# Kernel tuning notes

Hardware: AMD Instinct MI355X
Metric: run time of the kernel (lower is better)

The kernel has to match this reference:

```python
import jax, jax.numpy as jnp
import numpy as np

S, N, E = 4, 50000, 800000
DIM_C, DIM_H, HID = 8, 8, 32


def _mlp(x, W1, b1, W2, b2):
    # MLP(dim_in, dim_out, dim_hidden, num_hidden=1, CELU): lin -> celu -> lin
    return jax.nn.celu(x @ W1 + b1) @ W2 + b2


def setup_inputs() -> dict:
    key = jax.random.key(0)
    ks = jax.random.split(key, 12)

    def lin(k, fan_in, fan_out):
        kw, kb = jax.random.split(k)
        s = 1.0 / np.sqrt(fan_in)
        W = jax.random.uniform(kw, (fan_in, fan_out), jnp.float32, -s, s)
        b = jax.random.uniform(kb, (fan_out,), jnp.float32, -s, s)
        return W, b

    dz = DIM_C + DIM_H
    cur_W1, cur_b1 = lin(ks[0], dz, HID)
    cur_W2, cur_b2 = lin(ks[1], HID, HID)
    nbr_W1, nbr_b1 = lin(ks[2], dz, HID)
    nbr_W2, nbr_b2 = lin(ks[3], HID, HID)
    out_W, out_b = lin(ks[4], 2 * HID, DIM_C)
    G_W1, G_b1 = lin(ks[5], DIM_C, HID)
    G_W2, G_b2 = lin(ks[6], HID, DIM_H)

    z = jax.random.normal(ks[7], (S, N, dz), jnp.float32)
    src = jax.random.randint(ks[8], (E,), 0, N, jnp.int32)
    dst = jax.random.randint(ks[9], (E,), 0, N, jnp.int32)
    t = jnp.zeros((1,), jnp.float32)

    return dict(t=t, z=z, src=src, dst=dst,
                cur_W1=cur_W1, cur_b1=cur_b1, cur_W2=cur_W2, cur_b2=cur_b2,
                nbr_W1=nbr_W1, nbr_b1=nbr_b1, nbr_W2=nbr_W2, nbr_b2=nbr_b2,
                out_W=out_W, out_b=out_b,
                G_W1=G_W1, G_b1=G_b1, G_W2=G_W2, G_b2=G_b2)


def reference(t, z, src, dst,
              cur_W1, cur_b1, cur_W2, cur_b2,
              nbr_W1, nbr_b1, nbr_W2, nbr_b2,
              out_W, out_b,
              G_W1, G_b1, G_W2, G_b2):
    # z: [S, N, dim_c + dim_h]
    c = z[..., :DIM_C]          # [S, N, dim_c]
    h = z[..., DIM_C:]          # [S, N, dim_h]

    # GCU: vcur = act(MLP(z_node)); vnbr = sum over neighbors of act(MLP(z_nbr))
    vcur = jax.nn.celu(_mlp(z, cur_W1, cur_b1, cur_W2, cur_b2))      # [S, N, HID]
    vnbr_all = jax.nn.celu(_mlp(z, nbr_W1, nbr_b1, nbr_W2, nbr_b2))  # [S, N, HID]
    # segment-sum neighbor messages over edge list (nodes with no neighbors get zeros)
    agg = jnp.zeros((S, N, HID), z.dtype).at[:, dst].add(vnbr_all[:, src])  # [S, N, HID]

    dc = jnp.tanh(jnp.concatenate([vcur, agg], axis=-1) @ out_W + out_b)   # [S, N, dim_c]
    # project dc onto the tangent space orthogonal to c (sphere constraint)
    dc = dc - (dc * c).sum(axis=2, keepdims=True) / (c * c).sum(axis=2, keepdims=True) * c

    # gated decay of h
    G = jax.nn.softplus(_mlp(c, G_W1, G_b1, G_W2, G_b2))  # [S, N, dim_h]
    dh = -G * h

    return jnp.concatenate([dc, dh], axis=2)
```

## Files before the change

kernel.cpp:

```cpp
#include <hip/hip_runtime.h>

#define S_ 4
#define N_ 50000
#define E_ 800000
#define DIM_C 8
#define DIM_H 8
#define HID 32
#define DZ 16
#define CAP 64
#define NPART 6250
#define ECHUNK 2048
#define NCHUNK ((E_ + ECHUNK - 1) / ECHUNK)

typedef unsigned int u32;
typedef unsigned short u16;
typedef __attribute__((ext_vector_type(8))) short short8;
typedef __attribute__((ext_vector_type(4))) float f32x4;

__device__ __forceinline__ float celu_f(float x) {
    return x > 0.f ? x : __expf(x) - 1.f;
}
__device__ __forceinline__ float tanh_f(float x) {
    float e = __expf(-2.f * fabsf(x));
    float r = (1.f - e) * __builtin_amdgcn_rcpf(1.f + e);
    return copysignf(r, x);
}
__device__ __forceinline__ float softplus_f(float x) {
    return fmaxf(x, 0.f) + __logf(1.f + __expf(-fabsf(x)));
}
__device__ __forceinline__ u16 f2bf(float f) {
    u32 x = __float_as_uint(f);
    return (u16)((x + 0x7fffu + ((x >> 16) & 1u)) >> 16);
}
__device__ __forceinline__ float bf2f(u16 v) {
    return __uint_as_float(((u32)v) << 16);
}

#define MFMA(a, b, c) __builtin_amdgcn_mfma_f32_16x16x32_bf16(a, b, c, 0, 0, 0)

#define CNT_IDX(n) ((size_t)(n) << 5)
#define CNT_INT4S (N_ * 32 / 4)

__global__ __launch_bounds__(256) void zero_prep_kernel(
    const float* __restrict__ cW1, const float* __restrict__ cW2,
    const float* __restrict__ nW1, const float* __restrict__ nW2,
    const float* __restrict__ gW1, const float* __restrict__ gW2,
    const float* __restrict__ oW,
    u16* __restrict__ frags, int* __restrict__ cnt)
{
    if (blockIdx.x >= 13) {
        u32 i = (blockIdx.x - 13) * 256 + threadIdx.x;
        if (i < CNT_INT4S) {
            int4 zz; zz.x = 0; zz.y = 0; zz.z = 0; zz.w = 0;
            ((int4*)cnt)[i] = zz;
        }
        return;
    }
    if (threadIdx.x >= 64) return;
    int tile = blockIdx.x;
    int lane = threadIdx.x;
    int cl = lane & 15, g = lane >> 4;
    #pragma unroll
    for (int j = 0; j < 8; ++j) {
        int k = 8 * g + j;
        float v = 0.f;
        switch (tile) {
            case 0:  v = (k < DZ)    ? cW1[k*HID + cl]      : 0.f; break;
            case 1:  v = (k < DZ)    ? cW1[k*HID + cl + 16] : 0.f; break;
            case 2:  v = cW2[k*HID + cl];                          break;
            case 3:  v = cW2[k*HID + cl + 16];                     break;
            case 4:  v = (k < DZ)    ? nW1[k*HID + cl]      : 0.f; break;
            case 5:  v = (k < DZ)    ? nW1[k*HID + cl + 16] : 0.f; break;
            case 6:  v = nW2[k*HID + cl];                          break;
            case 7:  v = nW2[k*HID + cl + 16];                     break;
            case 8:  v = (k < DIM_C) ? gW1[k*HID + cl]      : 0.f; break;
            case 9:  v = (k < DIM_C) ? gW1[k*HID + cl + 16] : 0.f; break;
            case 10: v = (cl < DIM_H)? gW2[k*DIM_H + cl]    : 0.f; break;
            case 11: v = (cl < DIM_C)? oW[k*DIM_C + cl]        : 0.f; break;
            case 12: v = (cl < DIM_C)? oW[(HID+k)*DIM_C + cl]  : 0.f; break;
        }
        frags[((size_t)tile * 64 + lane) * 8 + j] = f2bf(v);
    }
}

__global__ __launch_bounds__(256) void node_fill_kernel(
    const float* __restrict__ z, const u16* __restrict__ frags,
    const float* __restrict__ cb1, const float* __restrict__ cb2,
    const float* __restrict__ nb1, const float* __restrict__ nb2,
    const float* __restrict__ gb1, const float* __restrict__ gb2,
    const float* __restrict__ ob,
    u16* __restrict__ pcd, u16* __restrict__ ub,
    const int* __restrict__ src, const int* __restrict__ dst,
    int* __restrict__ cnt, u16* __restrict__ list)
{
    __shared__ __align__(16) u16 sh[4][16][40];

    int m = blockIdx.x >> 4;
    int j = blockIdx.x & 15;

    if (j < 8) {
        int plo = j * NPART, phi = plo + NPART;
        int e0 = m * ECHUNK + (int)threadIdx.x * 8;
        if (e0 < E_) {
            int4 da = *(const int4*)(dst + e0);
            int4 db = *(const int4*)(dst + e0 + 4);
            int4 sa = *(const int4*)(src + e0);
            int4 sb = *(const int4*)(src + e0 + 4);
            int dv[8] = {da.x, da.y, da.z, da.w, db.x, db.y, db.z, db.w};
            int sv[8] = {sa.x, sa.y, sa.z, sa.w, sb.x, sb.y, sb.z, sb.w};
            #pragma unroll
            for (int i = 0; i < 8; ++i) {
                int dn = dv[i];
                if (dn >= plo && dn < phi) {
                    int pos = atomicAdd(&cnt[CNT_IDX(dn)], 1);
                    if (pos < CAP) list[(size_t)dn * CAP + pos] = (u16)sv[i];
                }
            }
        }
        return;
    }

    int g = m * 8 + (j - 8);
    if (g >= 3125) return;
    int w    = threadIdx.x >> 6;
    int lane = threadIdx.x & 63;
    int s = w;
    int base = g * 16;

    int r  = lane & 15;
    int gg = lane >> 4;
    int k0 = 8 * gg;

    const short8* F = (const short8*)frags;
    short8 bW1c_lo = F[0*64+lane],  bW1c_hi = F[1*64+lane];
    short8 bW2c_lo = F[2*64+lane],  bW2c_hi = F[3*64+lane];
    short8 bW1n_lo = F[4*64+lane],  bW1n_hi = F[5*64+lane];
    short8 bW2n_lo = F[6*64+lane],  bW2n_hi = F[7*64+lane];
    short8 bG1_lo  = F[8*64+lane],  bG1_hi  = F[9*64+lane];
    short8 bG2_lo  = F[10*64+lane];
    short8 bOWc    = F[11*64+lane], bOWn    = F[12*64+lane];

    int cl = r;
    float bc1lo = cb1[cl], bc1hi = cb1[cl+16];
    float bc2lo = cb2[cl], bc2hi = cb2[cl+16];
    float bn1lo = nb1[cl], bn1hi = nb1[cl+16];
    float bn2lo = nb2[cl], bn2hi = nb2[cl+16];
    float bg1lo = gb1[cl], bg1hi = gb1[cl+16];
    float bg2v  = (cl < 8) ? gb2[cl] : 0.f;
    float obv   = (cl < 8) ? ob[cl]  : 0.f;

    const f32x4 zero4 = {0.f, 0.f, 0.f, 0.f};

    int rowbase = s * N_ + base;

    short8 a1 = {0,0,0,0,0,0,0,0};
    if (gg < 2) {
        const float* zp = z + (size_t)(rowbase + r) * DZ + k0;
        float4 x = *(const float4*)zp;
        float4 y = *(const float4*)(zp + 4);
        a1[0]=(short)f2bf(x.x); a1[1]=(short)f2bf(x.y); a1[2]=(short)f2bf(x.z); a1[3]=(short)f2bf(x.w);
        a1[4]=(short)f2bf(y.x); a1[5]=(short)f2bf(y.y); a1[6]=(short)f2bf(y.z); a1[7]=(short)f2bf(y.w);
    }

    {
        f32x4 d0 = MFMA(a1, bW1c_lo, zero4);
        f32x4 d1 = MFMA(a1, bW1c_hi, zero4);
        #pragma unroll
        for (int q = 0; q < 4; ++q) {
            sh[w][4*gg+q][cl]    = f2bf(celu_f(d0[q] + bc1lo));
            sh[w][4*gg+q][cl+16] = f2bf(celu_f(d1[q] + bc1hi));
        }
        short8 a2 = *(const short8*)&sh[w][r][k0];
        d0 = MFMA(a2, bW2c_lo, zero4);
        d1 = MFMA(a2, bW2c_hi, zero4);
        #pragma unroll
        for (int q = 0; q < 4; ++q) {
            sh[w][4*gg+q][cl]    = f2bf(celu_f(d0[q] + bc2lo));
            sh[w][4*gg+q][cl+16] = f2bf(celu_f(d1[q] + bc2hi));
        }
        short8 a2v = *(const short8*)&sh[w][r][k0];
        f32x4 dp = MFMA(a2v, bOWc, zero4);
        if (cl < 8) {
            #pragma unroll
            for (int q = 0; q < 4; ++q)
                sh[w][4*gg+q][32 + cl] = f2bf(dp[q] + obv);
        }
        if (gg == 0) {
            uint4 vv = *(const uint4*)&sh[w][r][32];
            *(uint4*)(pcd + (size_t)(base + r) * 64 + s * 16) = vv;
        }
    }

    {
        f32x4 d0 = MFMA(a1, bW1n_lo, zero4);
        f32x4 d1 = MFMA(a1, bW1n_hi, zero4);
        #pragma unroll
        for (int q = 0; q < 4; ++q) {
            sh[w][4*gg+q][cl]    = f2bf(celu_f(d0[q] + bn1lo));
            sh[w][4*gg+q][cl+16] = f2bf(celu_f(d1[q] + bn1hi));
        }
        short8 a2 = *(const short8*)&sh[w][r][k0];
        d0 = MFMA(a2, bW2n_lo, zero4);
        d1 = MFMA(a2, bW2n_hi, zero4);
        #pragma unroll
        for (int q = 0; q < 4; ++q) {
            sh[w][4*gg+q][cl]    = f2bf(celu_f(d0[q] + bn2lo));
            sh[w][4*gg+q][cl+16] = f2bf(celu_f(d1[q] + bn2hi));
        }
        short8 a2n = *(const short8*)&sh[w][r][k0];
        f32x4 du = MFMA(a2n, bOWn, zero4);
        if (cl < 8) {
            #pragma unroll
            for (int q = 0; q < 4; ++q)
                sh[w][4*gg+q][32 + cl] = f2bf(du[q]);
        }
        if (gg == 0) {
            uint4 vv = *(const uint4*)&sh[w][r][32];
            *(uint4*)(ub + (size_t)(base + r) * 32 + s * 8) = vv;
        }
    }

    {
        f32x4 d0 = MFMA(a1, bG1_lo, zero4);
        f32x4 d1 = MFMA(a1, bG1_hi, zero4);
        #pragma unroll
        for (int q = 0; q < 4; ++q) {
            sh[w][4*gg+q][cl]    = f2bf(celu_f(d0[q] + bg1lo));
            sh[w][4*gg+q][cl+16] = f2bf(celu_f(d1[q] + bg1hi));
        }
        short8 a2 = *(const short8*)&sh[w][r][k0];
        f32x4 dG = MFMA(a2, bG2_lo, zero4);
        if (cl < 8) {
            #pragma unroll
            for (int q = 0; q < 4; ++q) {
                int mm = rowbase + 4*gg + q;
                float gv = softplus_f(dG[q] + bg2v);
                float hs = z[(size_t)mm * DZ + DIM_C + cl];
                sh[w][4*gg+q][32 + cl] = f2bf(-gv * hs);
            }
        }
        if (gg == 0) {
            uint4 vv = *(const uint4*)&sh[w][r][32];
            *(uint4*)(pcd + (size_t)(base + r) * 64 + s * 16 + 8) = vv;
        }
    }
}

__global__ __launch_bounds__(256) void gather_final_kernel(
    const u16* __restrict__ list, const int* __restrict__ cnt,
    const u16* __restrict__ ub, const u16* __restrict__ pcd,
    const float* __restrict__ z,
    float* __restrict__ out)
{
    int n = blockIdx.x * 4 + (threadIdx.x >> 6);
    int lane = threadIdx.x & 63;
    if (n >= N_) return;
    int deg = cnt[CNT_IDX(n)];
    deg = deg < CAP ? deg : CAP;
    int lv = (int)list[(size_t)n * CAP + lane];
    int half = lane >> 5;
    int ll = lane & 31;

    float sum = 0.f;
    int e = 0;
    for (; e + 7 < deg; e += 8) {
        int m0 = e + half;
        int s0 = __shfl(lv, m0);
        int s1 = __shfl(lv, m0 + 2);
        int s2 = __shfl(lv, m0 + 4);
        int s3 = __shfl(lv, m0 + 6);
        sum += bf2f(ub[(size_t)s0 * 32 + ll]);
        sum += bf2f(ub[(size_t)s1 * 32 + ll]);
        sum += bf2f(ub[(size_t)s2 * 32 + ll]);
        sum += bf2f(ub[(size_t)s3 * 32 + ll]);
    }
    for (; e < deg; e += 2) {
        int me = e + half;
        int sn = __shfl(lv, me & 63);
        if (me < deg) sum += bf2f(ub[(size_t)sn * 32 + ll]);
    }
    sum += __shfl_xor(sum, 32);

    if (half == 0) {
        int s = ll >> 3, j = ll & 7;
        int row = s * N_ + n;
        float pre = bf2f(pcd[(size_t)n * 64 + s * 16 + j]) + sum;
        float dc = tanh_f(pre);
        float c = z[(size_t)row * DZ + j];
        float num = dc * c, den = c * c;
        num += __shfl_xor(num, 1); den += __shfl_xor(den, 1);
        num += __shfl_xor(num, 2); den += __shfl_xor(den, 2);
        num += __shfl_xor(num, 4); den += __shfl_xor(den, 4);
        float coef = num * __builtin_amdgcn_rcpf(den);
        out[(size_t)row * DZ + j] = fmaf(-coef, c, dc);
        out[(size_t)row * DZ + DIM_C + j] = bf2f(pcd[(size_t)n * 64 + s * 16 + 8 + j]);
    }
}

extern "C" void kernel_launch(void* const* d_in, const int* in_sizes, int n_in,
                              void* d_out, int out_size, void* d_ws, size_t ws_size,
                              hipStream_t stream) {
    const float* z      = (const float*)d_in[1];
    const int*   src    = (const int*)  d_in[2];
    const int*   dst    = (const int*)  d_in[3];
    const float* cur_W1 = (const float*)d_in[4];
    const float* cur_b1 = (const float*)d_in[5];
    const float* cur_W2 = (const float*)d_in[6];
    const float* cur_b2 = (const float*)d_in[7];
    const float* nbr_W1 = (const float*)d_in[8];
    const float* nbr_b1 = (const float*)d_in[9];
    const float* nbr_W2 = (const float*)d_in[10];
    const float* nbr_b2 = (const float*)d_in[11];
    const float* out_W  = (const float*)d_in[12];
    const float* out_b  = (const float*)d_in[13];
    const float* G_W1   = (const float*)d_in[14];
    const float* G_b1   = (const float*)d_in[15];
    const float* G_W2   = (const float*)d_in[16];
    const float* G_b2   = (const float*)d_in[17];
    float* out = (float*)d_out;

    u16* ub    = (u16*)d_ws;
    u16* pcd   = ub + (size_t)N_ * 32;
    u16* list  = pcd + (size_t)N_ * 64;
    int* cnt   = (int*)(list + (size_t)N_ * CAP);
    u16* frags = (u16*)(cnt + (size_t)N_ * 32);

    int ZB = 13 + (CNT_INT4S + 255) / 256;
    zero_prep_kernel<<<ZB, 256, 0, stream>>>(
        cur_W1, cur_W2, nbr_W1, nbr_W2, G_W1, G_W2, out_W, frags, cnt);

    node_fill_kernel<<<NCHUNK * 16, 256, 0, stream>>>(
        z, frags,
        cur_b1, cur_b2, nbr_b1, nbr_b2, G_b1, G_b2, out_b,
        pcd, ub, src, dst, cnt, list);

    gather_final_kernel<<<(N_ + 3) / 4, 256, 0, stream>>>(
        list, cnt, ub, pcd, z, out);
}
```

Measured before the change: 73.08 us.

## Pre-bucket edges by destination partition to avoid redundant per-partition edge scans

Adds an edge-compaction phase to the prep kernel that buckets each 2048-edge chunk by destination partition in shared memory and writes packed (local dst, src) words to a global staging buffer. The scatter blocks in node_fill now read only their partition's entries instead of all edges in the chunk eightfold. This cuts redundant src/dst reads and branch-filtered work, at the cost of an extra staging write/read and moving edge work into the earlier kernel. Buckets are capped at 512 entries, which silently drops edges if a partition overflows.

```diff
diff --git a/kernel.cpp b/kernel.cpp
--- a/kernel.cpp
+++ b/kernel.cpp
@@ -11,6 +11,8 @@
 #define NPART 6250
 #define ECHUNK 2048
 #define NCHUNK ((E_ + ECHUNK - 1) / ECHUNK)
+#define STCAP 512
+#define ZEROB ((N_ * 32 / 4 + 255) / 256)
 
 typedef unsigned int u32;
 typedef unsigned short u16;
@@ -41,45 +43,85 @@
 #define CNT_IDX(n) ((size_t)(n) << 5)
 #define CNT_INT4S (N_ * 32 / 4)
 
-__global__ __launch_bounds__(256) void zero_prep_kernel(
+__global__ __launch_bounds__(256) void zero_prep_compact_kernel(
     const float* __restrict__ cW1, const float* __restrict__ cW2,
     const float* __restrict__ nW1, const float* __restrict__ nW2,
     const float* __restrict__ gW1, const float* __restrict__ gW2,
     const float* __restrict__ oW,
-    u16* __restrict__ frags, int* __restrict__ cnt)
+    const int* __restrict__ src, const int* __restrict__ dst,
+    u16* __restrict__ frags, int* __restrict__ cnt,
+    u32* __restrict__ stage, int* __restrict__ acount)
 {
-    if (blockIdx.x >= 13) {
-        u32 i = (blockIdx.x - 13) * 256 + threadIdx.x;
+    __shared__ u32 buck[8][STCAP];
+    __shared__ int bcnt[8];
+    const int bid = blockIdx.x;
+    const int tid = threadIdx.x;
+
+    if (bid < 13) {
+        if (tid >= 64) return;
+        int tile = bid;
+        int cl = tid & 15, g = tid >> 4;
+        #pragma unroll
+        for (int j = 0; j < 8; ++j) {
+            int k = 8 * g + j;
+            float v = 0.f;
+            switch (tile) {
+                case 0:  v = (k < DZ)    ? cW1[k*HID + cl]      : 0.f; break;
+                case 1:  v = (k < DZ)    ? cW1[k*HID + cl + 16] : 0.f; break;
+                case 2:  v = cW2[k*HID + cl];                          break;
+                case 3:  v = cW2[k*HID + cl + 16];                     break;
+                case 4:  v = (k < DZ)    ? nW1[k*HID + cl]      : 0.f; break;
+                case 5:  v = (k < DZ)    ? nW1[k*HID + cl + 16] : 0.f; break;
+                case 6:  v = nW2[k*HID + cl];                          break;
+                case 7:  v = nW2[k*HID + cl + 16];                     break;
+                case 8:  v = (k < DIM_C) ? gW1[k*HID + cl]      : 0.f; break;
+                case 9:  v = (k < DIM_C) ? gW1[k*HID + cl + 16] : 0.f; break;
+                case 10: v = (cl < DIM_H)? gW2[k*DIM_H + cl]    : 0.f; break;
+                case 11: v = (cl < DIM_C)? oW[k*DIM_C + cl]        : 0.f; break;
+                case 12: v = (cl < DIM_C)? oW[(HID+k)*DIM_C + cl]  : 0.f; break;
+            }
+            frags[((size_t)tile * 64 + tid) * 8 + j] = f2bf(v);
+        }
+        return;
+    }
+
+    if (bid < 13 + ZEROB) {
+        u32 i = (u32)(bid - 13) * 256 + tid;
         if (i < CNT_INT4S) {
             int4 zz; zz.x = 0; zz.y = 0; zz.z = 0; zz.w = 0;
             ((int4*)cnt)[i] = zz;
         }
         return;
     }
-    if (threadIdx.x >= 64) return;
-    int tile = blockIdx.x;
-    int lane = threadIdx.x;
-    int cl = lane & 15, g = lane >> 4;
+
+    int m = bid - (13 + ZEROB);
+    if (tid < 8) bcnt[tid] = 0;
+    __syncthreads();
+    int e0 = m * ECHUNK + tid * 8;
+    if (e0 < E_) {
+        int4 da = *(const int4*)(dst + e0);
+        int4 db = *(const int4*)(dst + e0 + 4);
+        int4 sa = *(const int4*)(src + e0);
+        int4 sb = *(const int4*)(src + e0 + 4);
+        int dv[8] = {da.x, da.y, da.z, da.w, db.x, db.y, db.z, db.w};
+        int sv[8] = {sa.x, sa.y, sa.z, sa.w, sb.x, sb.y, sb.z, sb.w};
+        #pragma unroll
+        for (int i = 0; i < 8; ++i) {
+            int dn = dv[i];
+            int p = dn / NPART;
+            int slot = atomicAdd(&bcnt[p], 1);
+            if (slot < STCAP)
+                buck[p][slot] = (u32)(dn - p * NPART) | ((u32)sv[i] << 16);
+        }
+    }
+    __syncthreads();
     #pragma unroll
-    for (int j = 0; j < 8; ++j) {
-        int k = 8 * g + j;
-        float v = 0.f;
-        switch (tile) {
-            case 0:  v = (k < DZ)    ? cW1[k*HID + cl]      : 0.f; break;
-            case 1:  v = (k < DZ)    ? cW1[k*HID + cl + 16] : 0.f; break;
-            case 2:  v = cW2[k*HID + cl];                          break;
-            case 3:  v = cW2[k*HID + cl + 16];                     break;
-            case 4:  v = (k < DZ)    ? nW1[k*HID + cl]      : 0.f; break;
-            case 5:  v = (k < DZ)    ? nW1[k*HID + cl + 16] : 0.f; break;
-            case 6:  v = nW2[k*HID + cl];                          break;
-            case 7:  v = nW2[k*HID + cl + 16];                     break;
-            case 8:  v = (k < DIM_C) ? gW1[k*HID + cl]      : 0.f; break;
-            case 9:  v = (k < DIM_C) ? gW1[k*HID + cl + 16] : 0.f; break;
-            case 10: v = (cl < DIM_H)? gW2[k*DIM_H + cl]    : 0.f; break;
-            case 11: v = (cl < DIM_C)? oW[k*DIM_C + cl]        : 0.f; break;
-            case 12: v = (cl < DIM_C)? oW[(HID+k)*DIM_C + cl]  : 0.f; break;
-        }
-        frags[((size_t)tile * 64 + lane) * 8 + j] = f2bf(v);
+    for (int p = 0; p < 8; ++p) {
+        int c = bcnt[p];
+        c = c < STCAP ? c : STCAP;
+        u32* sg = stage + ((size_t)m * 8 + p) * STCAP;
+        for (int i = tid; i < c; i += 256) sg[i] = buck[p][i];
+        if (tid == 0) acount[m * 8 + p] = c;
     }
 }
 
@@ -90,7 +132,7 @@
     const float* __restrict__ gb1, const float* __restrict__ gb2,
     const float* __restrict__ ob,
     u16* __restrict__ pcd, u16* __restrict__ ub,
-    const int* __restrict__ src, const int* __restrict__ dst,
+    const u32* __restrict__ stage, const int* __restrict__ acount,
     int* __restrict__ cnt, u16* __restrict__ list)
 {
     __shared__ __align__(16) u16 sh[4][16][40];
@@ -99,23 +141,15 @@
     int j = blockIdx.x & 15;
 
     if (j < 8) {
-        int plo = j * NPART, phi = plo + NPART;
-        int e0 = m * ECHUNK + (int)threadIdx.x * 8;
-        if (e0 < E_) {
-            int4 da = *(const int4*)(dst + e0);
-            int4 db = *(const int4*)(dst + e0 + 4);
-            int4 sa = *(const int4*)(src + e0);
-            int4 sb = *(const int4*)(src + e0 + 4);
-            int dv[8] = {da.x, da.y, da.z, da.w, db.x, db.y, db.z, db.w};
-            int sv[8] = {sa.x, sa.y, sa.z, sa.w, sb.x, sb.y, sb.z, sb.w};
-            #pragma unroll
-            for (int i = 0; i < 8; ++i) {
-                int dn = dv[i];
-                if (dn >= plo && dn < phi) {
-                    int pos = atomicAdd(&cnt[CNT_IDX(dn)], 1);
-                    if (pos < CAP) list[(size_t)dn * CAP + pos] = (u16)sv[i];
-                }
-            }
+        int c = acount[m * 8 + j];
+        int plo = j * NPART;
+        const u32* sg = stage + ((size_t)m * 8 + j) * STCAP;
+        for (int i = threadIdx.x; i < c; i += 256) {
+            u32 pk = sg[i];
+            int dn = plo + (int)(pk & 0xffffu);
+            int sn = (int)(pk >> 16);
+            int pos = atomicAdd(&cnt[CNT_IDX(dn)], 1);
+            if (pos < CAP) list[(size_t)dn * CAP + pos] = (u16)sn;
         }
         return;
     }
@@ -319,20 +353,23 @@
     const float* G_b2   = (const float*)d_in[17];
     float* out = (float*)d_out;
 
-    u16* ub    = (u16*)d_ws;
-    u16* pcd   = ub + (size_t)N_ * 32;
-    u16* list  = pcd + (size_t)N_ * 64;
-    int* cnt   = (int*)(list + (size_t)N_ * CAP);
-    u16* frags = (u16*)(cnt + (size_t)N_ * 32);
-
-    int ZB = 13 + (CNT_INT4S + 255) / 256;
-    zero_prep_kernel<<<ZB, 256, 0, stream>>>(
-        cur_W1, cur_W2, nbr_W1, nbr_W2, G_W1, G_W2, out_W, frags, cnt);
+    u16* ub     = (u16*)d_ws;
+    u16* pcd    = ub + (size_t)N_ * 32;
+    u16* list   = pcd + (size_t)N_ * 64;
+    int* cnt    = (int*)(list + (size_t)N_ * CAP);
+    u32* stage  = (u32*)(cnt + (size_t)N_ * 32);
+    int* acount = (int*)(stage + (size_t)NCHUNK * 8 * STCAP);
+    u16* frags  = (u16*)(acount + NCHUNK * 8);
+
+    int ZB = 13 + ZEROB + NCHUNK;
+    zero_prep_compact_kernel<<<ZB, 256, 0, stream>>>(
+        cur_W1, cur_W2, nbr_W1, nbr_W2, G_W1, G_W2, out_W,
+        src, dst, frags, cnt, stage, acount);
 
     node_fill_kernel<<<NCHUNK * 16, 256, 0, stream>>>(
         z, frags,
         cur_b1, cur_b2, nbr_b1, nbr_b2, G_b1, G_b2, out_b,
-        pcd, ub, src, dst, cnt, list);
+        pcd, ub, stage, acount, cnt, list);
 
     gather_final_kernel<<<(N_ + 3) / 4, 256, 0, stream>>>(
         list, cnt, ub, pcd, z, out);
```

Result: faster. 68.63 us (median of 2 runs) (-6.1%).
